# Performance work log

Measured on AMD Instinct MI355X. Metric: run time of the kernel, lower is better.

Reference implementation:

```python
import jax, jax.numpy as jnp
import numpy as np

B, N, H = 4096, 64, 256  # batch, num variables (input_dim == output_dim), hidden_dim
EPS = 1e-5  # nn.LayerNorm default eps


def setup_inputs() -> dict:
    key = jax.random.key(0)
    ks = jax.random.split(key, 10)
    s = lambda k, shape: jax.random.normal(k, shape, dtype=jnp.float32) * 0.05
    return {
        "x": jax.random.normal(ks[0], (B, N), dtype=jnp.float32),
        # flattened GRN: GRN(input_dim=N, hidden_dim=H, output_dim=N)
        "f_fc1_w": s(ks[1], (N, H)), "f_fc1_b": jnp.zeros((H,), jnp.float32),
        "f_fc2_w": s(ks[2], (H, N)), "f_fc2_b": jnp.zeros((N,), jnp.float32),
        "f_skip_w": s(ks[3], (N, N)), "f_skip_b": jnp.zeros((N,), jnp.float32),
        "f_gate_w": s(ks[4], (N, N)), "f_gate_b": jnp.zeros((N,), jnp.float32),
        "f_ln_g": jnp.ones((N,), jnp.float32), "f_ln_b": jnp.zeros((N,), jnp.float32),
        # per-variable GRNs: N copies of GRN(input_dim=1, hidden_dim=H, output_dim=H)
        "g_fc1_w": s(ks[5], (N, H)), "g_fc1_b": jnp.zeros((N, H), jnp.float32),
        "g_fc2_w": s(ks[6], (N, H, H)), "g_fc2_b": jnp.zeros((N, H), jnp.float32),
        "g_skip_w": s(ks[7], (N, H)), "g_skip_b": jnp.zeros((N, H), jnp.float32),
        "g_gate_w": s(ks[8], (N, H)), "g_gate_b": jnp.zeros((N, H), jnp.float32),
        "g_ln_g": jnp.ones((N, H), jnp.float32), "g_ln_b": jnp.zeros((N, H), jnp.float32),
    }


def _layer_norm(x, g, b):
    mu = jnp.mean(x, axis=-1, keepdims=True)
    var = jnp.mean(jnp.square(x - mu), axis=-1, keepdims=True)
    return (x - mu) * jax.lax.rsqrt(var + EPS) * g + b


def reference(x,
              f_fc1_w, f_fc1_b, f_fc2_w, f_fc2_b, f_skip_w, f_skip_b,
              f_gate_w, f_gate_b, f_ln_g, f_ln_b,
              g_fc1_w, g_fc1_b, g_fc2_w, g_fc2_b, g_skip_w, g_skip_b,
              g_gate_w, g_gate_b, g_ln_g, g_ln_b):
    # ---- flattened GRN: GRN(N -> H -> N); dropout is identity in eval mode ----
    h = jax.nn.elu(x @ f_fc1_w + f_fc1_b) @ f_fc2_w + f_fc2_b          # [B, N]
    skip = x @ f_skip_w + f_skip_b                                      # [B, N]
    gate = jax.nn.sigmoid(x @ f_gate_w + f_gate_b)                      # [B, N]
    w = _layer_norm(gate * h + (1.0 - gate) * skip, f_ln_g, f_ln_b)     # [B, N]
    sparse_w = jax.nn.softmax(w, axis=-1)                               # [B, N]

    # ---- per-variable GRNs (input_dim=1 -> hidden H), vectorized over the N variables ----
    xe = x[:, :, None]                                                  # [B, N, 1]
    hv = jax.nn.elu(xe * g_fc1_w + g_fc1_b)                             # [B, N, H] (fc1: 1->H)
    hv = jnp.einsum('bnh,nhk->bnk', hv, g_fc2_w) + g_fc2_b              # [B, N, H] (fc2: H->H per var)
    skv = xe * g_skip_w + g_skip_b                                      # [B, N, H] (skip: 1->H)
    gv = jax.nn.sigmoid(xe * g_gate_w + g_gate_b)                       # [B, N, H] (gate: 1->H)
    emb = _layer_norm(gv * hv + (1.0 - gv) * skv, g_ln_g, g_ln_b)       # [B, N, H]

    # softmax-weighted sum over the variable axis
    combined = jnp.sum(sparse_w[:, :, None] * emb, axis=1)              # [B, H]
    return combined, sparse_w[:, :, None]
```

## Files before the change

kernel.cpp:

```cpp
#include <hip/hip_runtime.h>
#include <hip/hip_bf16.h>

typedef __attribute__((ext_vector_type(4))) float f32x4;
typedef __attribute__((ext_vector_type(8))) short s16x8;

#define W2P_BYTES   8388608ull
#define SLAB_FLOATS 1048576ull
#define WS_NEEDED   (W2P_BYTES + 7ull * SLAB_FLOATS * 4ull)

__global__ __launch_bounds__(256) void k0_pack(const float* __restrict__ w2,
                                               ushort* __restrict__ out) {
  __shared__ float tile[32][257];
  const int n = blockIdx.x >> 3, ks = blockIdx.x & 7;
  const float* src = w2 + ((size_t)n * 256 + ks * 32) * 256;
  for (int i = threadIdx.x; i < 8192; i += 256)
    tile[i >> 8][i & 255] = src[i];
  __syncthreads();
#pragma unroll
  for (int q = 0; q < 4; ++q) {
    int chunk = q * 256 + threadIdx.x;
    int ct = chunk >> 6, l = chunk & 63;
    int g = l >> 4, cl = l & 15;
    s16x8 pk;
#pragma unroll
    for (int j = 0; j < 8; ++j) {
      __hip_bfloat16 h = __float2bfloat16(tile[g * 8 + j][ct * 16 + cl]);
      pk[j] = *reinterpret_cast<short*>(&h);
    }
    *reinterpret_cast<s16x8*>(out + ((size_t)(n * 8 + ks) * 1024 + chunk) * 8) = pk;
  }
}

__global__ __launch_bounds__(256) void k1_select(
    const float* __restrict__ x,
    const float* __restrict__ w1, const float* __restrict__ b1,
    const float* __restrict__ w2, const float* __restrict__ b2,
    const float* __restrict__ wsk, const float* __restrict__ bsk,
    const float* __restrict__ wg, const float* __restrict__ bg,
    const float* __restrict__ lng, const float* __restrict__ lnb,
    float* __restrict__ spw) {
  __shared__ float xs[8][64];
  __shared__ float t1[8][256];
  __shared__ float wvv[8][64];
  const int t = threadIdx.x;
  const int b0 = blockIdx.x * 8;
  if (t < 128) {
    const f32x4* xin = reinterpret_cast<const f32x4*>(x + (size_t)b0 * 64);
    reinterpret_cast<f32x4*>(&xs[0][0])[t] = xin[t];
  }
  __syncthreads();
  {
    float acc[8];
    float bias = b1[t];
#pragma unroll
    for (int r = 0; r < 8; ++r) acc[r] = bias;
    for (int n = 0; n < 64; ++n) {
      float w = w1[n * 256 + t];
#pragma unroll
      for (int r = 0; r < 8; ++r) acc[r] = fmaf(xs[r][n], w, acc[r]);
    }
#pragma unroll
    for (int r = 0; r < 8; ++r) {
      float z = acc[r];
      t1[r][t] = fmaxf(z, 0.f) + (__expf(fminf(z, 0.f)) - 1.f);
    }
  }
  __syncthreads();
  {
    const int nn = t & 63, rg = t >> 6;
    float a2[2], as_[2], ag[2];
    float bb2 = b2[nn], bbs = bsk[nn], bbg = bg[nn];
#pragma unroll
    for (int i = 0; i < 2; ++i) { a2[i] = bb2; as_[i] = bbs; ag[i] = bbg; }
    for (int h = 0; h < 256; ++h) {
      float w = w2[h * 64 + nn];
#pragma unroll
      for (int i = 0; i < 2; ++i) a2[i] = fmaf(t1[rg + 4 * i][h], w, a2[i]);
    }
    for (int m = 0; m < 64; ++m) {
      float ws_ = wsk[m * 64 + nn], wg_ = wg[m * 64 + nn];
#pragma unroll
      for (int i = 0; i < 2; ++i) {
        float xv = xs[rg + 4 * i][m];
        as_[i] = fmaf(xv, ws_, as_[i]);
        ag[i]  = fmaf(xv, wg_, ag[i]);
      }
    }
#pragma unroll
    for (int i = 0; i < 2; ++i) {
      float gt = __fdividef(1.f, 1.f + __expf(-ag[i]));
      wvv[rg + 4 * i][nn] = fmaf(gt, a2[i] - as_[i], as_[i]);
    }
  }
  __syncthreads();
  {
    const int lane = t & 63, wid = t >> 6;
    float gl = lng[lane], bl = lnb[lane];
#pragma unroll
    for (int rr = 0; rr < 2; ++rr) {
      int r = wid * 2 + rr;
      float v = wvv[r][lane];
      float s = v;
      for (int m = 1; m < 64; m <<= 1) s += __shfl_xor(s, m);
      float mu = s * (1.f / 64.f);
      float d = v - mu;
      float q = d * d;
      for (int m = 1; m < 64; m <<= 1) q += __shfl_xor(q, m);
      float wn = d * rsqrtf(q * (1.f / 64.f) + 1e-5f) * gl + bl;
      float mx = wn;
      for (int m = 1; m < 64; m <<= 1) mx = fmaxf(mx, __shfl_xor(mx, m));
      float e = __expf(wn - mx);
      float se = e;
      for (int m = 1; m < 64; m <<= 1) se += __shfl_xor(se, m);
      spw[(size_t)(b0 + r) * 64 + lane] = __fdividef(e, se);
    }
  }
}

template <bool ATOMIC>
__global__ __launch_bounds__(512, 4) void k2_main(
    const float* __restrict__ x,
    const ushort* __restrict__ w2p,
    const float* __restrict__ fc1w, const float* __restrict__ fc1b,
    const float* __restrict__ fc2b,
    const float* __restrict__ skw, const float* __restrict__ skb,
    const float* __restrict__ gww, const float* __restrict__ gwb,
    const float* __restrict__ lng, const float* __restrict__ lnb,
    const float* __restrict__ spw,
    float* __restrict__ comb, float* __restrict__ slabs) {
  __shared__ __align__(16) char Ab[16384];
  __shared__ __align__(16) float pbuf[2][1792];
  __shared__ float xs[32][9];
  __shared__ float ss[32][9];
  __shared__ float sums[2][32][2];

  const int bid = blockIdx.x;
  const int nch = bid & 7;
  const int b0  = (bid >> 3) * 32;
  const int t = threadIdx.x;
  const int lane = t & 63;
  const int w = t >> 6;
  const int g = lane >> 4;
  const int cl = lane & 15;
  const int n0 = nch * 8;

  if (t < 256) {
    int r = t >> 3, j = t & 7;
    xs[r][j] = x[(size_t)(b0 + r) * 64 + nch * 8 + j];
    ss[r][j] = spw[(size_t)(b0 + r) * 64 + nch * 8 + j];
  }
  if (t < 64) (&sums[0][0][0])[t] = 0.f;

  auto STAGE = [&](int nn, int buf) {
    if (w < 7) {
      const float* ps;
      switch (w) {
        case 0: ps = fc2b; break;
        case 1: ps = skw;  break;
        case 2: ps = skb;  break;
        case 3: ps = gww;  break;
        case 4: ps = gwb;  break;
        case 5: ps = lng;  break;
        default: ps = lnb; break;
      }
      __builtin_amdgcn_global_load_lds(
          (const __attribute__((address_space(1))) unsigned int*)(ps + nn * 256 + lane * 4),
          (__attribute__((address_space(3))) unsigned int*)&pbuf[buf][w * 256],
          16, 0, 0);
    }
  };

  f32x4 comb_acc[2][2];
#pragma unroll
  for (int a = 0; a < 2; ++a)
#pragma unroll
    for (int b = 0; b < 2; ++b) comb_acc[a][b] = (f32x4){0.f, 0.f, 0.f, 0.f};

  const s16x8* wf = reinterpret_cast<const s16x8*>(w2p);
#define BFRAG(nn, kk, ct) \
  (wf + (((size_t)((nn) * 8 + (kk)) * 16 + w * 2 + (ct)) * 64 + lane))

  STAGE(n0, 0);
  __syncthreads();

  for (int ni = 0; ni < 8; ++ni) {
    const int n = n0 + ni;
    s16x8 bfa[2], bfb[2];
#pragma unroll
    for (int ct = 0; ct < 2; ++ct) {
      bfa[ct] = *BFRAG(n, 0, ct);
      bfb[ct] = *BFRAG(n, 1, ct);
    }

    {
      const int kc = t & 31;
      const int rb = t >> 5;
      const float* w1p = fc1w + n * 256 + kc * 8;
      const float* b1p = fc1b + n * 256 + kc * 8;
      f32x4 wlo = *reinterpret_cast<const f32x4*>(w1p);
      f32x4 whi = *reinterpret_cast<const f32x4*>(w1p + 4);
      f32x4 blo = *reinterpret_cast<const f32x4*>(b1p);
      f32x4 bhi = *reinterpret_cast<const f32x4*>(b1p + 4);
#pragma unroll
      for (int i = 0; i < 2; ++i) {
        int r = rb + 16 * i;
        float xv = xs[r][ni];
        s16x8 pk;
#pragma unroll
        for (int j = 0; j < 4; ++j) {
          float z0 = fmaf(xv, wlo[j], blo[j]);
          float z1 = fmaf(xv, whi[j], bhi[j]);
          float e0 = fmaxf(z0, 0.f) + (__expf(fminf(z0, 0.f)) - 1.f);
          float e1 = fmaxf(z1, 0.f) + (__expf(fminf(z1, 0.f)) - 1.f);
          __hip_bfloat16 h0 = __float2bfloat16(e0);
          __hip_bfloat16 h1 = __float2bfloat16(e1);
          pk[j]     = *reinterpret_cast<short*>(&h0);
          pk[j + 4] = *reinterpret_cast<short*>(&h1);
        }
        *reinterpret_cast<s16x8*>(Ab + r * 512 + ((kc << 4) ^ ((r & 7) << 4))) = pk;
      }
    }
    __syncthreads();

    if (ni < 7) STAGE(n + 1, (ni + 1) & 1);

    f32x4 acc[2][2];
#pragma unroll
    for (int a = 0; a < 2; ++a)
#pragma unroll
      for (int b = 0; b < 2; ++b) acc[a][b] = (f32x4){0.f, 0.f, 0.f, 0.f};

#pragma unroll
    for (int ks = 0; ks < 8; ++ks) {
      s16x8* cur = (ks & 1) ? bfb : bfa;
      s16x8 af[2];
#pragma unroll
      for (int rt = 0; rt < 2; ++rt) {
        int row = rt * 16 + cl;
        af[rt] = *reinterpret_cast<const s16x8*>(
            Ab + row * 512 + (((ks * 4 + g) << 4) ^ ((row & 7) << 4)));
      }
#pragma unroll
      for (int ct = 0; ct < 2; ++ct)
#pragma unroll
        for (int rt = 0; rt < 2; ++rt)
          acc[ct][rt] = __builtin_amdgcn_mfma_f32_16x16x32_bf16(
              cur[ct], af[rt], acc[ct][rt], 0, 0, 0);
      if (ks < 6) {
#pragma unroll
        for (int ct = 0; ct < 2; ++ct) cur[ct] = *BFRAG(n, ks + 2, ct);
      }
    }

    const int par = ni & 1;
    const float* pb = &pbuf[ni & 1][0];
    {
      float xr[2], rsum[2], rsq[2];
#pragma unroll
      for (int rt = 0; rt < 2; ++rt) {
        xr[rt] = xs[rt * 16 + cl][ni];
        rsum[rt] = 0.f;
        rsq[rt] = 0.f;
      }
#pragma unroll
      for (int ct = 0; ct < 2; ++ct) {
        const int cl4 = (w * 2 + ct) * 16 + g * 4;
        f32x4 f2b4 = *reinterpret_cast<const f32x4*>(pb + 0 * 256 + cl4);
        f32x4 sw4  = *reinterpret_cast<const f32x4*>(pb + 1 * 256 + cl4);
        f32x4 sb4  = *reinterpret_cast<const f32x4*>(pb + 2 * 256 + cl4);
        f32x4 gw4  = *reinterpret_cast<const f32x4*>(pb + 3 * 256 + cl4);
        f32x4 gb4  = *reinterpret_cast<const f32x4*>(pb + 4 * 256 + cl4);
#pragma unroll
        for (int rt = 0; rt < 2; ++rt) {
#pragma unroll
          for (int j = 0; j < 4; ++j) {
            float hv = acc[ct][rt][j] + f2b4[j];
            float sk = fmaf(xr[rt], sw4[j], sb4[j]);
            float gv = __fdividef(1.f, 1.f + __expf(-fmaf(xr[rt], gw4[j], gb4[j])));
            float p = fmaf(gv, hv - sk, sk);
            acc[ct][rt][j] = p;
            rsum[rt] += p;
            rsq[rt] = fmaf(p, p, rsq[rt]);
          }
        }
      }
#pragma unroll
      for (int rt = 0; rt < 2; ++rt) {
        rsum[rt] += __shfl_xor(rsum[rt], 16);
        rsum[rt] += __shfl_xor(rsum[rt], 32);
        rsq[rt]  += __shfl_xor(rsq[rt], 16);
        rsq[rt]  += __shfl_xor(rsq[rt], 32);
      }
      if (g == 0) {
#pragma unroll
        for (int rt = 0; rt < 2; ++rt) {
          atomicAdd(&sums[par][rt * 16 + cl][0], rsum[rt]);
          atomicAdd(&sums[par][rt * 16 + cl][1], rsq[rt]);
        }
      }
    }
    if (t < 64) (&sums[par ^ 1][0][0])[t] = 0.f;
    __syncthreads();

    {
      float rsv[2], mrs[2], svv[2];
#pragma unroll
      for (int rt = 0; rt < 2; ++rt) {
        int row = rt * 16 + cl;
        float s0 = sums[par][row][0], s1 = sums[par][row][1];
        float mu = s0 * (1.f / 256.f);
        float rs = rsqrtf(fmaxf(s1 * (1.f / 256.f) - mu * mu, 0.f) + 1e-5f);
        rsv[rt] = rs;
        mrs[rt] = -mu * rs;
        svv[rt] = ss[row][ni];
      }
#pragma unroll
      for (int ct = 0; ct < 2; ++ct) {
        const int cl4 = (w * 2 + ct) * 16 + g * 4;
        f32x4 lg4 = *reinterpret_cast<const f32x4*>(pb + 5 * 256 + cl4);
        f32x4 lb4 = *reinterpret_cast<const f32x4*>(pb + 6 * 256 + cl4);
#pragma unroll
        for (int rt = 0; rt < 2; ++rt) {
#pragma unroll
          for (int j = 0; j < 4; ++j) {
            float tnorm = fmaf(acc[ct][rt][j], rsv[rt], mrs[rt]);
            float emb = fmaf(tnorm, lg4[j], lb4[j]);
            comb_acc[ct][rt][j] = fmaf(svv[rt], emb, comb_acc[ct][rt][j]);
          }
        }
      }
    }
  }
#undef BFRAG

  float* outp;
  if (ATOMIC) outp = comb;
  else outp = (nch == 0) ? comb : slabs + (size_t)(nch - 1) * SLAB_FLOATS;
#pragma unroll
  for (int ct = 0; ct < 2; ++ct)
#pragma unroll
    for (int rt = 0; rt < 2; ++rt) {
      size_t idx = (size_t)(b0 + rt * 16 + cl) * 256 + (w * 2 + ct) * 16 + g * 4;
      if (ATOMIC) {
#pragma unroll
        for (int j = 0; j < 4; ++j)
          atomicAdd(&outp[idx + j], comb_acc[ct][rt][j]);
      } else {
        *reinterpret_cast<f32x4*>(outp + idx) = comb_acc[ct][rt];
      }
    }
}

__global__ __launch_bounds__(256) void k3_reduce(float* __restrict__ comb,
                                                 const float* __restrict__ slabs) {
  size_t i = (size_t)blockIdx.x * 256 + threadIdx.x;
  f32x4 v = reinterpret_cast<const f32x4*>(comb)[i];
#pragma unroll
  for (int s = 0; s < 7; ++s)
    v += reinterpret_cast<const f32x4*>(slabs)[s * (SLAB_FLOATS / 4) + i];
  reinterpret_cast<f32x4*>(comb)[i] = v;
}

extern "C" void kernel_launch(void* const* d_in, const int* in_sizes, int n_in,
                              void* d_out, int out_size, void* d_ws, size_t ws_size,
                              hipStream_t stream) {
  const float* x   = (const float*)d_in[0];
  const float* f1w = (const float*)d_in[1];
  const float* f1b = (const float*)d_in[2];
  const float* f2w = (const float*)d_in[3];
  const float* f2b = (const float*)d_in[4];
  const float* fsw = (const float*)d_in[5];
  const float* fsb = (const float*)d_in[6];
  const float* fgw = (const float*)d_in[7];
  const float* fgb = (const float*)d_in[8];
  const float* flg = (const float*)d_in[9];
  const float* flb = (const float*)d_in[10];
  const float* g1w = (const float*)d_in[11];
  const float* g1b = (const float*)d_in[12];
  const float* g2w = (const float*)d_in[13];
  const float* g2b = (const float*)d_in[14];
  const float* gsw = (const float*)d_in[15];
  const float* gsb = (const float*)d_in[16];
  const float* ggw = (const float*)d_in[17];
  const float* ggb = (const float*)d_in[18];
  const float* glg = (const float*)d_in[19];
  const float* glb = (const float*)d_in[20];

  float* out  = (float*)d_out;
  float* comb = out;
  float* spw  = out + (size_t)4096 * 256;
  ushort* w2p = (ushort*)d_ws;
  float* slabs = (float*)((char*)d_ws + W2P_BYTES);

  k0_pack<<<512, 256, 0, stream>>>(g2w, w2p);
  k1_select<<<512, 256, 0, stream>>>(x, f1w, f1b, f2w, f2b, fsw, fsb,
                                     fgw, fgb, flg, flb, spw);
  if (ws_size >= WS_NEEDED) {
    k2_main<false><<<1024, 512, 0, stream>>>(x, w2p, g1w, g1b, g2b, gsw, gsb,
                                             ggw, ggb, glg, glb, spw, comb, slabs);
    k3_reduce<<<1024, 256, 0, stream>>>(comb, slabs);
  } else {
    hipMemsetAsync(comb, 0, (size_t)4096 * 256 * sizeof(float), stream);
    k2_main<true><<<1024, 512, 0, stream>>>(x, w2p, g1w, g1b, g2b, gsw, gsb,
                                            ggw, ggb, glg, glb, spw, comb, slabs);
  }
}
```

Baseline: 136.4 us.

## Merge pack and select kernels; software-pipeline A-gen and LayerNorm pass in main kernel

Fuses the weight-pack kernel and the selection-GRN kernel into one launch, splitting the work by block index, so one launch and its tail are removed. In the main kernel, the A operand buffer is double-buffered and the param/sum buffers are triple-buffered. The next variable's fc1/ELU A tile is generated, and the previous variable's LayerNorm/accumulate pass is done, around the current MFMA work, so each iteration needs one barrier instead of two. This raises LDS use and keeps the acc registers live across iterations, which may lower occupancy under launch_bounds(512,4).

```diff
diff --git a/kernel.cpp b/kernel.cpp
--- a/kernel.cpp
+++ b/kernel.cpp
@@ -8,30 +8,8 @@
 #define SLAB_FLOATS 1048576ull
 #define WS_NEEDED   (W2P_BYTES + 7ull * SLAB_FLOATS * 4ull)
 
-__global__ __launch_bounds__(256) void k0_pack(const float* __restrict__ w2,
-                                               ushort* __restrict__ out) {
-  __shared__ float tile[32][257];
-  const int n = blockIdx.x >> 3, ks = blockIdx.x & 7;
-  const float* src = w2 + ((size_t)n * 256 + ks * 32) * 256;
-  for (int i = threadIdx.x; i < 8192; i += 256)
-    tile[i >> 8][i & 255] = src[i];
-  __syncthreads();
-#pragma unroll
-  for (int q = 0; q < 4; ++q) {
-    int chunk = q * 256 + threadIdx.x;
-    int ct = chunk >> 6, l = chunk & 63;
-    int g = l >> 4, cl = l & 15;
-    s16x8 pk;
-#pragma unroll
-    for (int j = 0; j < 8; ++j) {
-      __hip_bfloat16 h = __float2bfloat16(tile[g * 8 + j][ct * 16 + cl]);
-      pk[j] = *reinterpret_cast<short*>(&h);
-    }
-    *reinterpret_cast<s16x8*>(out + ((size_t)(n * 8 + ks) * 1024 + chunk) * 8) = pk;
-  }
-}
-
-__global__ __launch_bounds__(256) void k1_select(
+__global__ __launch_bounds__(256) void k01(
+    const float* __restrict__ g2w, ushort* __restrict__ out,
     const float* __restrict__ x,
     const float* __restrict__ w1, const float* __restrict__ b1,
     const float* __restrict__ w2, const float* __restrict__ b2,
@@ -39,80 +17,103 @@
     const float* __restrict__ wg, const float* __restrict__ bg,
     const float* __restrict__ lng, const float* __restrict__ lnb,
     float* __restrict__ spw) {
-  __shared__ float xs[8][64];
-  __shared__ float t1[8][256];
-  __shared__ float wvv[8][64];
+  __shared__ __align__(16) float shbuf[32 * 257];
   const int t = threadIdx.x;
-  const int b0 = blockIdx.x * 8;
-  if (t < 128) {
-    const f32x4* xin = reinterpret_cast<const f32x4*>(x + (size_t)b0 * 64);
-    reinterpret_cast<f32x4*>(&xs[0][0])[t] = xin[t];
-  }
-  __syncthreads();
-  {
-    float acc[8];
-    float bias = b1[t];
-#pragma unroll
-    for (int r = 0; r < 8; ++r) acc[r] = bias;
-    for (int n = 0; n < 64; ++n) {
-      float w = w1[n * 256 + t];
-#pragma unroll
-      for (int r = 0; r < 8; ++r) acc[r] = fmaf(xs[r][n], w, acc[r]);
-    }
-#pragma unroll
-    for (int r = 0; r < 8; ++r) {
-      float z = acc[r];
-      t1[r][t] = fmaxf(z, 0.f) + (__expf(fminf(z, 0.f)) - 1.f);
-    }
-  }
-  __syncthreads();
-  {
-    const int nn = t & 63, rg = t >> 6;
-    float a2[2], as_[2], ag[2];
-    float bb2 = b2[nn], bbs = bsk[nn], bbg = bg[nn];
-#pragma unroll
-    for (int i = 0; i < 2; ++i) { a2[i] = bb2; as_[i] = bbs; ag[i] = bbg; }
-    for (int h = 0; h < 256; ++h) {
-      float w = w2[h * 64 + nn];
-#pragma unroll
-      for (int i = 0; i < 2; ++i) a2[i] = fmaf(t1[rg + 4 * i][h], w, a2[i]);
-    }
-    for (int m = 0; m < 64; ++m) {
-      float ws_ = wsk[m * 64 + nn], wg_ = wg[m * 64 + nn];
+  if (blockIdx.x < 512) {
+    float (*tile)[257] = reinterpret_cast<float (*)[257]>(shbuf);
+    const int n = blockIdx.x >> 3, ks = blockIdx.x & 7;
+    const float* src = g2w + ((size_t)n * 256 + ks * 32) * 256;
+    for (int i = t; i < 8192; i += 256)
+      tile[i >> 8][i & 255] = src[i];
+    __syncthreads();
+#pragma unroll
+    for (int q = 0; q < 4; ++q) {
+      int chunk = q * 256 + t;
+      int ct = chunk >> 6, l = chunk & 63;
+      int g = l >> 4, cl = l & 15;
+      s16x8 pk;
+#pragma unroll
+      for (int j = 0; j < 8; ++j) {
+        __hip_bfloat16 h = __float2bfloat16(tile[g * 8 + j][ct * 16 + cl]);
+        pk[j] = *reinterpret_cast<short*>(&h);
+      }
+      *reinterpret_cast<s16x8*>(out + ((size_t)(n * 8 + ks) * 1024 + chunk) * 8) = pk;
+    }
+  } else {
+    float (*xs)[64]  = reinterpret_cast<float (*)[64]>(shbuf);
+    float (*t1)[256] = reinterpret_cast<float (*)[256]>(shbuf + 512);
+    float (*wvv)[64] = reinterpret_cast<float (*)[64]>(shbuf + 2560);
+    const int b0 = (int)(blockIdx.x - 512) * 8;
+    if (t < 128) {
+      const f32x4* xin = reinterpret_cast<const f32x4*>(x + (size_t)b0 * 64);
+      reinterpret_cast<f32x4*>(&xs[0][0])[t] = xin[t];
+    }
+    __syncthreads();
+    {
+      float acc[8];
+      float bias = b1[t];
+#pragma unroll
+      for (int r = 0; r < 8; ++r) acc[r] = bias;
+      for (int n = 0; n < 64; ++n) {
+        float w = w1[n * 256 + t];
+#pragma unroll
+        for (int r = 0; r < 8; ++r) acc[r] = fmaf(xs[r][n], w, acc[r]);
+      }
+#pragma unroll
+      for (int r = 0; r < 8; ++r) {
+        float z = acc[r];
+        t1[r][t] = fmaxf(z, 0.f) + (__expf(fminf(z, 0.f)) - 1.f);
+      }
+    }
+    __syncthreads();
+    {
+      const int nn = t & 63, rg = t >> 6;
+      float a2[2], as_[2], ag[2];
+      float bb2 = b2[nn], bbs = bsk[nn], bbg = bg[nn];
+#pragma unroll
+      for (int i = 0; i < 2; ++i) { a2[i] = bb2; as_[i] = bbs; ag[i] = bbg; }
+      for (int h = 0; h < 256; ++h) {
+        float w = w2[h * 64 + nn];
+#pragma unroll
+        for (int i = 0; i < 2; ++i) a2[i] = fmaf(t1[rg + 4 * i][h], w, a2[i]);
+      }
+      for (int m = 0; m < 64; ++m) {
+        float ws_ = wsk[m * 64 + nn], wg_ = wg[m * 64 + nn];
+#pragma unroll
+        for (int i = 0; i < 2; ++i) {
+          float xv = xs[rg + 4 * i][m];
+          as_[i] = fmaf(xv, ws_, as_[i]);
+          ag[i]  = fmaf(xv, wg_, ag[i]);
+        }
+      }
 #pragma unroll
       for (int i = 0; i < 2; ++i) {
-        float xv = xs[rg + 4 * i][m];
-        as_[i] = fmaf(xv, ws_, as_[i]);
-        ag[i]  = fmaf(xv, wg_, ag[i]);
-      }
-    }
-#pragma unroll
-    for (int i = 0; i < 2; ++i) {
-      float gt = __fdividef(1.f, 1.f + __expf(-ag[i]));
-      wvv[rg + 4 * i][nn] = fmaf(gt, a2[i] - as_[i], as_[i]);
-    }
-  }
-  __syncthreads();
-  {
-    const int lane = t & 63, wid = t >> 6;
-    float gl = lng[lane], bl = lnb[lane];
-#pragma unroll
-    for (int rr = 0; rr < 2; ++rr) {
-      int r = wid * 2 + rr;
-      float v = wvv[r][lane];
-      float s = v;
-      for (int m = 1; m < 64; m <<= 1) s += __shfl_xor(s, m);
-      float mu = s * (1.f / 64.f);
-      float d = v - mu;
-      float q = d * d;
-      for (int m = 1; m < 64; m <<= 1) q += __shfl_xor(q, m);
-      float wn = d * rsqrtf(q * (1.f / 64.f) + 1e-5f) * gl + bl;
-      float mx = wn;
-      for (int m = 1; m < 64; m <<= 1) mx = fmaxf(mx, __shfl_xor(mx, m));
-      float e = __expf(wn - mx);
-      float se = e;
-      for (int m = 1; m < 64; m <<= 1) se += __shfl_xor(se, m);
-      spw[(size_t)(b0 + r) * 64 + lane] = __fdividef(e, se);
+        float gt = __fdividef(1.f, 1.f + __expf(-ag[i]));
+        wvv[rg + 4 * i][nn] = fmaf(gt, a2[i] - as_[i], as_[i]);
+      }
+    }
+    __syncthreads();
+    {
+      const int lane = t & 63, wid = t >> 6;
+      float gl = lng[lane], bl = lnb[lane];
+#pragma unroll
+      for (int rr = 0; rr < 2; ++rr) {
+        int r = wid * 2 + rr;
+        float v = wvv[r][lane];
+        float s = v;
+        for (int m = 1; m < 64; m <<= 1) s += __shfl_xor(s, m);
+        float mu = s * (1.f / 64.f);
+        float d = v - mu;
+        float q = d * d;
+        for (int m = 1; m < 64; m <<= 1) q += __shfl_xor(q, m);
+        float wn = d * rsqrtf(q * (1.f / 64.f) + 1e-5f) * gl + bl;
+        float mx = wn;
+        for (int m = 1; m < 64; m <<= 1) mx = fmaxf(mx, __shfl_xor(mx, m));
+        float e = __expf(wn - mx);
+        float se = e;
+        for (int m = 1; m < 64; m <<= 1) se += __shfl_xor(se, m);
+        spw[(size_t)(b0 + r) * 64 + lane] = __fdividef(e, se);
+      }
     }
   }
 }
@@ -128,11 +129,11 @@
     const float* __restrict__ lng, const float* __restrict__ lnb,
     const float* __restrict__ spw,
     float* __restrict__ comb, float* __restrict__ slabs) {
-  __shared__ __align__(16) char Ab[16384];
-  __shared__ __align__(16) float pbuf[2][1792];
+  __shared__ __align__(16) char Ab[2][16384];
+  __shared__ __align__(16) float pbuf[3][1792];
   __shared__ float xs[32][9];
   __shared__ float ss[32][9];
-  __shared__ float sums[2][32][2];
+  __shared__ float sums[3][32][2];
 
   const int bid = blockIdx.x;
   const int nch = bid & 7;
@@ -170,21 +171,87 @@
     }
   };
 
+  auto AGEN = [&](int nn, char* abuf) {
+    const int kc = t & 31;
+    const int rb = t >> 5;
+    const int nloc = nn - n0;
+    const float* w1p = fc1w + nn * 256 + kc * 8;
+    const float* b1p = fc1b + nn * 256 + kc * 8;
+    f32x4 wlo = *reinterpret_cast<const f32x4*>(w1p);
+    f32x4 whi = *reinterpret_cast<const f32x4*>(w1p + 4);
+    f32x4 blo = *reinterpret_cast<const f32x4*>(b1p);
+    f32x4 bhi = *reinterpret_cast<const f32x4*>(b1p + 4);
+#pragma unroll
+    for (int i = 0; i < 2; ++i) {
+      int r = rb + 16 * i;
+      float xv = xs[r][nloc];
+      s16x8 pk;
+#pragma unroll
+      for (int j = 0; j < 4; ++j) {
+        float z0 = fmaf(xv, wlo[j], blo[j]);
+        float z1 = fmaf(xv, whi[j], bhi[j]);
+        float e0 = fmaxf(z0, 0.f) + (__expf(fminf(z0, 0.f)) - 1.f);
+        float e1 = fmaxf(z1, 0.f) + (__expf(fminf(z1, 0.f)) - 1.f);
+        __hip_bfloat16 h0 = __float2bfloat16(e0);
+        __hip_bfloat16 h1 = __float2bfloat16(e1);
+        pk[j]     = *reinterpret_cast<short*>(&h0);
+        pk[j + 4] = *reinterpret_cast<short*>(&h1);
+      }
+      *reinterpret_cast<s16x8*>(abuf + r * 512 + ((kc << 4) ^ ((r & 7) << 4))) = pk;
+    }
+  };
+
   f32x4 comb_acc[2][2];
+  f32x4 acc[2][2];
 #pragma unroll
   for (int a = 0; a < 2; ++a)
 #pragma unroll
     for (int b = 0; b < 2; ++b) comb_acc[a][b] = (f32x4){0.f, 0.f, 0.f, 0.f};
+
+  auto PASS2 = [&](int pni) {
+    const float* sb = &sums[pni % 3][0][0];
+    const float* pb = &pbuf[pni % 3][0];
+    float rsv[2], mrs[2], svv[2];
+#pragma unroll
+    for (int rt = 0; rt < 2; ++rt) {
+      int row = rt * 16 + cl;
+      float s0 = sb[row * 2], s1 = sb[row * 2 + 1];
+      float mu = s0 * (1.f / 256.f);
+      float rs = rsqrtf(fmaxf(s1 * (1.f / 256.f) - mu * mu, 0.f) + 1e-5f);
+      rsv[rt] = rs;
+      mrs[rt] = -mu * rs;
+      svv[rt] = ss[row][pni];
+    }
+#pragma unroll
+    for (int ct = 0; ct < 2; ++ct) {
+      const int cl4 = (w * 2 + ct) * 16 + g * 4;
+      f32x4 lg4 = *reinterpret_cast<const f32x4*>(pb + 5 * 256 + cl4);
+      f32x4 lb4 = *reinterpret_cast<const f32x4*>(pb + 6 * 256 + cl4);
+#pragma unroll
+      for (int rt = 0; rt < 2; ++rt) {
+#pragma unroll
+        for (int j = 0; j < 4; ++j) {
+          float tnorm = fmaf(acc[ct][rt][j], rsv[rt], mrs[rt]);
+          float emb = fmaf(tnorm, lg4[j], lb4[j]);
+          comb_acc[ct][rt][j] = fmaf(svv[rt], emb, comb_acc[ct][rt][j]);
+        }
+      }
+    }
+  };
 
   const s16x8* wf = reinterpret_cast<const s16x8*>(w2p);
 #define BFRAG(nn, kk, ct) \
   (wf + (((size_t)((nn) * 8 + (kk)) * 16 + w * 2 + (ct)) * 64 + lane))
 
+  __syncthreads();
   STAGE(n0, 0);
+  AGEN(n0, Ab[0]);
   __syncthreads();
 
   for (int ni = 0; ni < 8; ++ni) {
     const int n = n0 + ni;
+    if (t < 64) (&sums[(ni + 1) % 3][0][0])[t] = 0.f;
+
     s16x8 bfa[2], bfb[2];
 #pragma unroll
     for (int ct = 0; ct < 2; ++ct) {
@@ -192,44 +259,16 @@
       bfb[ct] = *BFRAG(n, 1, ct);
     }
 
-    {
-      const int kc = t & 31;
-      const int rb = t >> 5;
-      const float* w1p = fc1w + n * 256 + kc * 8;
-      const float* b1p = fc1b + n * 256 + kc * 8;
-      f32x4 wlo = *reinterpret_cast<const f32x4*>(w1p);
-      f32x4 whi = *reinterpret_cast<const f32x4*>(w1p + 4);
-      f32x4 blo = *reinterpret_cast<const f32x4*>(b1p);
-      f32x4 bhi = *reinterpret_cast<const f32x4*>(b1p + 4);
-#pragma unroll
-      for (int i = 0; i < 2; ++i) {
-        int r = rb + 16 * i;
-        float xv = xs[r][ni];
-        s16x8 pk;
-#pragma unroll
-        for (int j = 0; j < 4; ++j) {
-          float z0 = fmaf(xv, wlo[j], blo[j]);
-          float z1 = fmaf(xv, whi[j], bhi[j]);
-          float e0 = fmaxf(z0, 0.f) + (__expf(fminf(z0, 0.f)) - 1.f);
-          float e1 = fmaxf(z1, 0.f) + (__expf(fminf(z1, 0.f)) - 1.f);
-          __hip_bfloat16 h0 = __float2bfloat16(e0);
-          __hip_bfloat16 h1 = __float2bfloat16(e1);
-          pk[j]     = *reinterpret_cast<short*>(&h0);
-          pk[j + 4] = *reinterpret_cast<short*>(&h1);
-        }
-        *reinterpret_cast<s16x8*>(Ab + r * 512 + ((kc << 4) ^ ((r & 7) << 4))) = pk;
-      }
-    }
-    __syncthreads();
-
-    if (ni < 7) STAGE(n + 1, (ni + 1) & 1);
-
-    f32x4 acc[2][2];
+    if (ni > 0) PASS2(ni - 1);
+
+    if (ni < 7) STAGE(n + 1, (ni + 1) % 3);
+
 #pragma unroll
     for (int a = 0; a < 2; ++a)
 #pragma unroll
       for (int b = 0; b < 2; ++b) acc[a][b] = (f32x4){0.f, 0.f, 0.f, 0.f};
 
+    const char* abase = Ab[ni & 1];
 #pragma unroll
     for (int ks = 0; ks < 8; ++ks) {
       s16x8* cur = (ks & 1) ? bfb : bfa;
@@ -238,7 +277,7 @@
       for (int rt = 0; rt < 2; ++rt) {
         int row = rt * 16 + cl;
         af[rt] = *reinterpret_cast<const s16x8*>(
-            Ab + row * 512 + (((ks * 4 + g) << 4) ^ ((row & 7) << 4)));
+            abase + row * 512 + (((ks * 4 + g) << 4) ^ ((row & 7) << 4)));
       }
 #pragma unroll
       for (int ct = 0; ct < 2; ++ct)
@@ -252,9 +291,8 @@
       }
     }
 
-    const int par = ni & 1;
-    const float* pb = &pbuf[ni & 1][0];
     {
+      const float* pb = &pbuf[ni % 3][0];
       float xr[2], rsum[2], rsq[2];
 #pragma unroll
       for (int rt = 0; rt < 2; ++rt) {
@@ -292,45 +330,21 @@
         rsq[rt]  += __shfl_xor(rsq[rt], 32);
       }
       if (g == 0) {
+        float* sb2 = &sums[ni % 3][0][0];
 #pragma unroll
         for (int rt = 0; rt < 2; ++rt) {
-          atomicAdd(&sums[par][rt * 16 + cl][0], rsum[rt]);
-          atomicAdd(&sums[par][rt * 16 + cl][1], rsq[rt]);
+          atomicAdd(&sb2[(rt * 16 + cl) * 2 + 0], rsum[rt]);
+          atomicAdd(&sb2[(rt * 16 + cl) * 2 + 1], rsq[rt]);
         }
       }
     }
-    if (t < 64) (&sums[par ^ 1][0][0])[t] = 0.f;
+
+    if (ni < 7) AGEN(n + 1, Ab[(ni + 1) & 1]);
+
     __syncthreads();
-
-    {
-      float rsv[2], mrs[2], svv[2];
-#pragma unroll
-      for (int rt = 0; rt < 2; ++rt) {
-        int row = rt * 16 + cl;
-        float s0 = sums[par][row][0], s1 = sums[par][row][1];
-        float mu = s0 * (1.f / 256.f);
-        float rs = rsqrtf(fmaxf(s1 * (1.f / 256.f) - mu * mu, 0.f) + 1e-5f);
-        rsv[rt] = rs;
-        mrs[rt] = -mu * rs;
-        svv[rt] = ss[row][ni];
-      }
-#pragma unroll
-      for (int ct = 0; ct < 2; ++ct) {
-        const int cl4 = (w * 2 + ct) * 16 + g * 4;
-        f32x4 lg4 = *reinterpret_cast<const f32x4*>(pb + 5 * 256 + cl4);
-        f32x4 lb4 = *reinterpret_cast<const f32x4*>(pb + 6 * 256 + cl4);
-#pragma unroll
-        for (int rt = 0; rt < 2; ++rt) {
-#pragma unroll
-          for (int j = 0; j < 4; ++j) {
-            float tnorm = fmaf(acc[ct][rt][j], rsv[rt], mrs[rt]);
-            float emb = fmaf(tnorm, lg4[j], lb4[j]);
-            comb_acc[ct][rt][j] = fmaf(svv[rt], emb, comb_acc[ct][rt][j]);
-          }
-        }
-      }
-    }
   }
+
+  PASS2(7);
 #undef BFRAG
 
   float* outp;
@@ -392,9 +406,8 @@
   ushort* w2p = (ushort*)d_ws;
   float* slabs = (float*)((char*)d_ws + W2P_BYTES);
 
-  k0_pack<<<512, 256, 0, stream>>>(g2w, w2p);
-  k1_select<<<512, 256, 0, stream>>>(x, f1w, f1b, f2w, f2b, fsw, fsb,
-                                     fgw, fgb, flg, flb, spw);
+  k01<<<1024, 256, 0, stream>>>(g2w, w2p, x, f1w, f1b, f2w, f2b,
+                                fsw, fsb, fgw, fgb, flg, flb, spw);
   if (ws_size >= WS_NEEDED) {
     k2_main<false><<<1024, 512, 0, stream>>>(x, w2p, g1w, g1b, g2b, gsw, gsb,
                                              ggw, ggb, glg, glb, spw, comb, slabs);
```

New measurement: 129.6 us, median of 3. 5.0% less time.
